# Performance work log

Measured on AMD Instinct MI355X. Metric: run time of the kernel, lower is better.

## Reference

```python
import jax, jax.numpy as jnp
import numpy as np

N_SKILL = 50000
B = 4096          # number of (job, resume) pairs; n_job == n_resume required by the concat
E = 65536         # edges per relation (avg degree 16)
D = 1536          # embedding_dim
HID = [512, 256, 64]


def setup_inputs() -> dict:
    key = jax.random.key(0)
    ks = jax.random.split(key, 16)
    nrm = lambda k, shape, s=0.02: jax.random.normal(k, shape, dtype=jnp.float32) * s
    inp = {
        "x_skill": jax.random.normal(ks[0], (N_SKILL, D), dtype=jnp.float32),
        "x_job": jax.random.normal(ks[1], (B, D), dtype=jnp.float32),
        "x_resume": jax.random.normal(ks[2], (B, D), dtype=jnp.float32),
        "src_sj": jax.random.randint(ks[3], (E,), 0, N_SKILL),
        "dst_sj": jax.random.randint(ks[4], (E,), 0, B),
        "src_sr": jax.random.randint(ks[5], (E,), 0, N_SKILL),
        "dst_sr": jax.random.randint(ks[6], (E,), 0, B),
        "W_rel_j": nrm(ks[7], (D, D)),
        "b_rel_j": jnp.zeros((D,), jnp.float32),
        "W_root_j": nrm(ks[8], (D, D)),
        "W_rel_r": nrm(ks[9], (D, D)),
        "b_rel_r": jnp.zeros((D,), jnp.float32),
        "W_root_r": nrm(ks[10], (D, D)),
        "W1": nrm(ks[11], (2 * D, HID[0])), "b1": jnp.zeros((HID[0],), jnp.float32),
        "W2": nrm(ks[12], (HID[0], HID[1])), "b2": jnp.zeros((HID[1],), jnp.float32),
        "W3": nrm(ks[13], (HID[1], HID[2])), "b3": jnp.zeros((HID[2],), jnp.float32),
        "W4": nrm(ks[14], (HID[2], 1)), "b4": jnp.zeros((1,), jnp.float32),
    }
    return inp


def _graph_conv(x_src, x_dst, src, dst, W_rel, b_rel, W_root):
    # PyG GraphConv (aggr='add', bipartite): out = lin_rel(sum_{j in N(i)} x_j) + lin_root(x_i)
    agg = jax.ops.segment_sum(x_src[src], dst, num_segments=x_dst.shape[0])  # [B, D]
    return agg @ W_rel + b_rel + x_dst @ W_root


def reference(x_skill, x_job, x_resume, src_sj, dst_sj, src_sr, dst_sr,
              W_rel_j, b_rel_j, W_root_j, W_rel_r, b_rel_r, W_root_r,
              W1, b1, W2, b2, W3, b3, W4, b4):
    # HeteroConv: each dst node type ('job', 'resume') receives exactly one relation,
    # so the cross-relation 'mean' aggregation is the identity.
    h_job = jax.nn.relu(_graph_conv(x_skill, x_job, src_sj, dst_sj, W_rel_j, b_rel_j, W_root_j))
    h_res = jax.nn.relu(_graph_conv(x_skill, x_resume, src_sr, dst_sr, W_rel_r, b_rel_r, W_root_r))
    h = jnp.concatenate([h_job, h_res], axis=1)  # [B, 2D]
    # MLP (dropout is inference-mode identity)
    h = jax.nn.relu(h @ W1 + b1)
    h = jax.nn.relu(h @ W2 + b2)
    h = jax.nn.relu(h @ W3 + b3)
    score = (h @ W4 + b4).squeeze(-1)  # [B]
    return score
```

## Files before the change

### kernel.cpp

```cpp
#include <hip/hip_runtime.h>

#define E_EDGES 65536
#define NB 4096
#define DD 1536
#define CAP 96

typedef unsigned short u16;
typedef __bf16 bf16x8 __attribute__((ext_vector_type(8)));
typedef float f32x4 __attribute__((ext_vector_type(4)));

#define AS1(p) ((const __attribute__((address_space(1))) void*)(p))
#define AS3(p) ((__attribute__((address_space(3))) void*)(p))

__device__ __forceinline__ u16 f2bf(float f) {
    unsigned u = __float_as_uint(f);
    u += 0x7fffu + ((u >> 16) & 1u);
    return (u16)(u >> 16);
}


__global__ __launch_bounds__(256) void bucket_kernel(
    const int* __restrict__ sj, const int* __restrict__ dj,
    const int* __restrict__ sr, const int* __restrict__ dr,
    int* __restrict__ cnt, int* __restrict__ bkt) {
    int e = blockIdx.x * 256 + threadIdx.x;
    int rel = blockIdx.y;
    int s = rel ? sr[e] : sj[e];
    int d = rel ? dr[e] : dj[e];
    int slot = rel * NB + d;
    int pos = atomicAdd(&cnt[slot], 1);
    if (pos < CAP) bkt[(size_t)slot * CAP + pos] = s;
}


__global__ __launch_bounds__(128) void agg_cvt_kernel(
    const float* __restrict__ xskill, const float* __restrict__ xj, const float* __restrict__ xr,
    const int* __restrict__ bkt, const int* __restrict__ cnt,
    u16* __restrict__ Aj, u16* __restrict__ Ar) {
    int rel = blockIdx.y;
    int row = blockIdx.x;
    int t = threadIdx.x;
    const float* xd = (rel ? xr : xj) + (size_t)row * DD;
    u16* A = (rel ? Ar : Aj) + (size_t)row * (2 * DD);

    float4 v[3];
#pragma unroll
    for (int c = 0; c < 3; ++c) v[c] = *(const float4*)(xd + t * 4 + c * 512);
#pragma unroll
    for (int c = 0; c < 3; ++c) {
        ushort4 o = {f2bf(v[c].x), f2bf(v[c].y), f2bf(v[c].z), f2bf(v[c].w)};
        *(ushort4*)(A + DD + t * 4 + c * 512) = o;
    }

    int count = cnt[rel * NB + row];
    if (count > CAP) count = CAP;
    __shared__ int sidx[CAP];
    if (t < count) sidx[t] = bkt[(size_t)(rel * NB + row) * CAP + t];
    __syncthreads();

    float4 acc[3] = {};
    for (int e = 0; e < count; ++e) {
        const float* xs = xskill + (size_t)sidx[e] * DD;
#pragma unroll
        for (int c = 0; c < 3; ++c) {
            float4 u = *(const float4*)(xs + t * 4 + c * 512);
            acc[c].x += u.x; acc[c].y += u.y; acc[c].z += u.z; acc[c].w += u.w;
        }
    }
#pragma unroll
    for (int c = 0; c < 3; ++c) {
        ushort4 o = {f2bf(acc[c].x), f2bf(acc[c].y), f2bf(acc[c].z), f2bf(acc[c].w)};
        *(ushort4*)(A + t * 4 + c * 512) = o;
    }
}


__global__ __launch_bounds__(256) void transpose_all(
    const float* __restrict__ w0, const float* __restrict__ w1,
    const float* __restrict__ w2, const float* __restrict__ w3,
    const float* __restrict__ w4, const float* __restrict__ w5,
    u16* __restrict__ Wjt, u16* __restrict__ Wrt,
    u16* __restrict__ W1t, u16* __restrict__ W2t) {
    int bid = blockIdx.x;
    const float* in; u16* out; int N, ldo, k0, nbx;
    if (bid < 9216) {
        int m = bid / 2304;
        bid = bid % 2304;
        in = (m == 0) ? w0 : (m == 1) ? w1 : (m == 2) ? w2 : w3;
        out = (m < 2) ? Wjt : Wrt;
        N = 1536; ldo = 3072; k0 = (m & 1) ? DD : 0; nbx = 48;
    } else if (bid < 10752) {
        bid -= 9216;
        in = w4; out = W1t; N = 512; ldo = 3072; k0 = 0; nbx = 16;
    } else {
        bid -= 10752;
        in = w5; out = W2t; N = 256; ldo = 512; k0 = 0; nbx = 8;
    }
    int bx = (bid % nbx) * 32;
    int by = (bid / nbx) * 32;
    __shared__ float tile[32][33];
    int tx = threadIdx.x & 31, ty = threadIdx.x >> 5;
#pragma unroll
    for (int i = 0; i < 4; ++i)
        tile[ty + i * 8][tx] = in[(size_t)(by + ty + i * 8) * N + bx + tx];
    __syncthreads();
#pragma unroll
    for (int i = 0; i < 4; ++i) {
        int n = bx + ty + i * 8;
        int k = by + tx;
        out[(size_t)n * ldo + k0 + k] = f2bf(tile[tx][ty + i * 8]);
    }
}


template <int BM, bool OUT_BF16, bool DUAL>
__global__ __launch_bounds__(256) void gemm_bias_relu(
    const u16* __restrict__ A0, const u16* __restrict__ Bt0, const float* __restrict__ bias0,
    const u16* __restrict__ A1, const u16* __restrict__ Bt1, const float* __restrict__ bias1,
    void* __restrict__ C, int K, int ldc) {
    constexpr int BK = 64;
    constexpr int MI = BM / 32;
    constexpr int NITER = (BM + 128) / 32;
    __shared__ u16 lA[BM * BK];
    __shared__ u16 lB[128 * BK];
    int tid = threadIdx.x;
    int lane = tid & 63;
    int w = tid >> 6;
    long bm = (long)blockIdx.x * BM;
    long bn = (long)blockIdx.y * 128;
    const u16* A = A0; const u16* Bt = Bt0; const float* bias = bias0;
    long col_ofs = 0;
    if (DUAL && blockIdx.z) { A = A1; Bt = Bt1; bias = bias1; col_ofs = DD; }
    int wm = (w >> 1) * (BM / 2), wn = (w & 1) * 64;
    f32x4 acc[MI][4] = {};
    const int lrow = lane & 15;
    const int lko = (lane >> 4) * 8;

    for (int k0 = 0; k0 < K; k0 += BK) {
#pragma unroll
        for (int i = 0; i < NITER; ++i) {
            int chunk = i * 256 + tid;
            int row = chunk >> 3, kc = chunk & 7;
            if (row < BM) {
                const u16* g = A + (bm + row) * (long)K + k0 + kc * 8;
                __builtin_amdgcn_global_load_lds(AS1(g), AS3((char*)lA + i * 4096 + w * 1024), 16, 0, 0);
            } else {
                const u16* g = Bt + (bn + row - BM) * (long)K + k0 + kc * 8;
                __builtin_amdgcn_global_load_lds(AS1(g), AS3((char*)lB + i * 4096 + w * 1024 - BM * 128), 16, 0, 0);
            }
        }
        __syncthreads();
#pragma unroll
        for (int kk = 0; kk < BK; kk += 32) {
            bf16x8 af[MI], bfr[4];
#pragma unroll
            for (int i = 0; i < MI; ++i)
                af[i] = *(const bf16x8*)(lA + (wm + i * 16 + lrow) * BK + kk + lko);
#pragma unroll
            for (int j = 0; j < 4; ++j)
                bfr[j] = *(const bf16x8*)(lB + (wn + j * 16 + lrow) * BK + kk + lko);
#pragma unroll
            for (int i = 0; i < MI; ++i)
#pragma unroll
                for (int j = 0; j < 4; ++j)
                    acc[i][j] = __builtin_amdgcn_mfma_f32_16x16x32_bf16(af[i], bfr[j], acc[i][j], 0, 0, 0);
        }
        __syncthreads();
    }

    int rb = (lane >> 4) * 4, cl = lane & 15;
#pragma unroll
    for (int i = 0; i < MI; ++i)
#pragma unroll
        for (int j = 0; j < 4; ++j) {
            long row = bm + wm + i * 16 + rb;
            long col = bn + wn + j * 16 + cl;
            float b = bias[col];
#pragma unroll
            for (int r = 0; r < 4; ++r) {
                float v = fmaxf(acc[i][j][r] + b, 0.f);
                long o = (row + r) * (long)ldc + col_ofs + col;
                if (OUT_BF16)
                    ((u16*)C)[o] = f2bf(v);
                else
                    ((float*)C)[o] = v;
            }
        }
}


__global__ __launch_bounds__(64) void l34_kernel(
    const float* __restrict__ h2, const float* __restrict__ W3, const float* __restrict__ b3,
    const float* __restrict__ W4, const float* __restrict__ b4, float* __restrict__ out) {
    int t = threadIdx.x;
    __shared__ float hrow[256];
    float w4t = W4[t];
    float b3t = b3[t];
    for (int rr = 0; rr < 4; ++rr) {
        int row = blockIdx.x * 4 + rr;
        __syncthreads();
        ((float4*)hrow)[t] = ((const float4*)(h2 + (size_t)row * 256))[t];
        __syncthreads();
        float acc = b3t;
#pragma unroll 8
        for (int k = 0; k < 256; ++k) acc = fmaf(hrow[k], W3[k * 64 + t], acc);
        acc = fmaxf(acc, 0.f);
        float s = acc * w4t;
#pragma unroll
        for (int o = 32; o > 0; o >>= 1) s += __shfl_down(s, o);
        if (t == 0) out[row] = s + b4[0];
    }
}


extern "C" void kernel_launch(void* const* d_in, const int* in_sizes, int n_in,
                              void* d_out, int out_size, void* d_ws, size_t ws_size,
                              hipStream_t stream) {
    (void)in_sizes; (void)n_in; (void)out_size; (void)ws_size;
    const float* x_skill  = (const float*)d_in[0];
    const float* x_job    = (const float*)d_in[1];
    const float* x_resume = (const float*)d_in[2];
    const int* src_sj = (const int*)d_in[3];
    const int* dst_sj = (const int*)d_in[4];
    const int* src_sr = (const int*)d_in[5];
    const int* dst_sr = (const int*)d_in[6];
    const float* W_rel_j  = (const float*)d_in[7];
    const float* b_rel_j  = (const float*)d_in[8];
    const float* W_root_j = (const float*)d_in[9];
    const float* W_rel_r  = (const float*)d_in[10];
    const float* b_rel_r  = (const float*)d_in[11];
    const float* W_root_r = (const float*)d_in[12];
    const float* W1 = (const float*)d_in[13];
    const float* b1 = (const float*)d_in[14];
    const float* W2 = (const float*)d_in[15];
    const float* b2 = (const float*)d_in[16];
    const float* W3 = (const float*)d_in[17];
    const float* b3 = (const float*)d_in[18];
    const float* W4 = (const float*)d_in[19];
    const float* b4 = (const float*)d_in[20];
    float* out = (float*)d_out;

    char* p = (char*)d_ws;
    auto alloc = [&](size_t bytes) -> char* {
        char* r = p;
        p += (bytes + 255) & ~(size_t)255;
        return r;
    };
    int* cnt = (int*)alloc(2 * NB * 4);
    int* bkt = (int*)alloc((size_t)2 * NB * CAP * 4);
    u16* Aj   = (u16*)alloc((size_t)NB * 2 * DD * 2);
    u16* Ar   = (u16*)alloc((size_t)NB * 2 * DD * 2);
    u16* Wjt  = (u16*)alloc((size_t)DD * 2 * DD * 2);
    u16* Wrt  = (u16*)alloc((size_t)DD * 2 * DD * 2);
    u16* W1t  = (u16*)alloc((size_t)512 * 3072 * 2);
    u16* W2t  = (u16*)alloc((size_t)256 * 512 * 2);
    u16* hcat = (u16*)alloc((size_t)NB * 3072 * 2);
    u16* h1   = (u16*)alloc((size_t)NB * 512 * 2);
    float* h2 = (float*)alloc((size_t)NB * 256 * 4);

    hipMemsetAsync(cnt, 0, 2 * NB * 4, stream);
    bucket_kernel<<<dim3(E_EDGES / 256, 2), 256, 0, stream>>>(src_sj, dst_sj, src_sr, dst_sr, cnt, bkt);
    transpose_all<<<10880, 256, 0, stream>>>(W_rel_j, W_root_j, W_rel_r, W_root_r, W1, W2,
                                             Wjt, Wrt, W1t, W2t);
    agg_cvt_kernel<<<dim3(NB, 2), 128, 0, stream>>>(x_skill, x_job, x_resume, bkt, cnt, Aj, Ar);

    gemm_bias_relu<128, true, true><<<dim3(NB / 128, DD / 128, 2), 256, 0, stream>>>(
        Aj, Wjt, b_rel_j, Ar, Wrt, b_rel_r, hcat, 3072, 3072);
    gemm_bias_relu<64, true, false><<<dim3(NB / 64, 512 / 128, 1), 256, 0, stream>>>(
        hcat, W1t, b1, nullptr, nullptr, nullptr, h1, 3072, 512);
    gemm_bias_relu<64, false, false><<<dim3(NB / 64, 256 / 128, 1), 256, 0, stream>>>(
        h1, W2t, b2, nullptr, nullptr, nullptr, h2, 512, 256);
    l34_kernel<<<NB / 4, 64, 0, stream>>>(h2, W3, b3, W4, b4, out);
}
```

Before: 366.2 us.

## Replace dual conv GEMM with 256x256-tile double-buffered pipelined kernel

Adds a dedicated conv GEMM kernel that uses 256x256 output tiles with 8 waves, double-buffered LDS staging, an XOR-swizzled LDS layout to avoid bank conflicts, and interleaved prefetch of the next K tile between MFMA phases using explicit vmcnt waits and barriers. It also remaps block IDs for better L2 locality. The goal is more data reuse per tile and overlap of global loads with the MFMAs in the dominant GEMM. In exchange it uses 128KB of LDS per block and many barriers, which limits occupancy and makes correctness depend on the hand-written waitcnt and barrier ordering.

```diff
diff --git a/kernel.cpp b/kernel.cpp
--- a/kernel.cpp
+++ b/kernel.cpp
@@ -11,6 +11,10 @@
 
 #define AS1(p) ((const __attribute__((address_space(1))) void*)(p))
 #define AS3(p) ((__attribute__((address_space(3))) void*)(p))
+
+#define BAR() do { __builtin_amdgcn_s_barrier(); asm volatile("" ::: "memory"); } while (0)
+#define VMCNT2() asm volatile("s_waitcnt vmcnt(2)" ::: "memory")
+#define VMCNT0() asm volatile("s_waitcnt vmcnt(0)" ::: "memory")
 
 __device__ __forceinline__ u16 f2bf(float f) {
     unsigned u = __float_as_uint(f);
@@ -113,10 +117,153 @@
 }
 
 
-template <int BM, bool OUT_BF16, bool DUAL>
+__global__ __launch_bounds__(512, 2) void conv_gemm256(
+    const u16* __restrict__ Aj, const u16* __restrict__ Wjt, const float* __restrict__ bj,
+    const u16* __restrict__ Ar, const u16* __restrict__ Wrt, const float* __restrict__ br,
+    u16* __restrict__ C) {
+    constexpr int K = 3072, NT = K / 64, LDC = 3072;
+    __shared__ u16 lds[65536];
+    int tid = threadIdx.x;
+    int lane = tid & 63;
+    int w = tid >> 6;
+
+    int bid = blockIdx.y * 16 + blockIdx.x;
+    bid = (bid & 7) * 12 + (bid >> 3);
+    long bm = (long)(bid % 16) * 256;
+    long bn = (long)(bid / 16) * 256;
+
+    const u16* A; const u16* Bt; const float* bias; long cofs;
+    if (blockIdx.z) { A = Ar; Bt = Wrt; bias = br; cofs = DD; }
+    else            { A = Aj; Bt = Wjt; bias = bj; cofs = 0;  }
+
+    int wm = (w >> 2) * 128;
+    int wn = (w & 3) * 64;
+
+    const int sr0 = (w * 2) * 8 + (lane >> 3);
+    const int sr1 = (w * 2 + 1) * 8 + (lane >> 3);
+    const int skf = ((lane & 7) * 8) ^ ((lane >> 3) << 3);
+
+    auto stageA = [&](int b, int h, long k0) {
+        const u16* g0 = A + (bm + h * 128 + sr0) * (long)K + k0 + skf;
+        const u16* g1 = A + (bm + h * 128 + sr1) * (long)K + k0 + skf;
+        __builtin_amdgcn_global_load_lds(AS1(g0), AS3(lds + b * 32768 + h * 8192 + (w * 2 + 0) * 512), 16, 0, 0);
+        __builtin_amdgcn_global_load_lds(AS1(g1), AS3(lds + b * 32768 + h * 8192 + (w * 2 + 1) * 512), 16, 0, 0);
+    };
+    auto stageB = [&](int b, int h, long k0) {
+        const u16* g0 = Bt + (bn + h * 128 + sr0) * (long)K + k0 + skf;
+        const u16* g1 = Bt + (bn + h * 128 + sr1) * (long)K + k0 + skf;
+        __builtin_amdgcn_global_load_lds(AS1(g0), AS3(lds + b * 32768 + 16384 + h * 8192 + (w * 2 + 0) * 512), 16, 0, 0);
+        __builtin_amdgcn_global_load_lds(AS1(g1), AS3(lds + b * 32768 + 16384 + h * 8192 + (w * 2 + 1) * 512), 16, 0, 0);
+    };
+
+    const int lrow = lane & 15;
+    const int lko = (lane >> 4) * 8;
+    const int rsw = (lane & 7) << 3;
+
+    auto ldA = [&](int b, int mi, int kk) -> bf16x8 {
+        return *(const bf16x8*)(lds + b * 32768 + (wm + mi * 16 + lrow) * 64 + ((kk + lko) ^ rsw));
+    };
+    auto ldB = [&](int b, int nj, int kk) -> bf16x8 {
+        return *(const bf16x8*)(lds + b * 32768 + 16384 + (wn + nj * 16 + lrow) * 64 + ((kk + lko) ^ rsw));
+    };
+
+    f32x4 acc[8][4] = {};
+    bf16x8 bfr[4];
+
+    stageA(0, 0, 0); stageA(0, 1, 0);
+    stageB(0, 0, 0); stageB(0, 1, 0);
+
+    for (int t = 0; t < NT; ++t) {
+        int b = t & 1;
+        long k1 = (long)(t + 1) * 64;
+        bool pf = (t + 1 < NT);
+
+        if (pf) { stageA(b ^ 1, 0, k1); VMCNT2(); } else { VMCNT0(); }
+        BAR();
+        {
+            bf16x8 af[4];
+#pragma unroll
+            for (int mi = 0; mi < 4; ++mi) af[mi] = ldA(b, mi, 0);
+#pragma unroll
+            for (int nj = 0; nj < 4; ++nj) bfr[nj] = ldB(b, nj, 0);
+            __builtin_amdgcn_s_setprio(1);
+#pragma unroll
+            for (int mi = 0; mi < 4; ++mi)
+#pragma unroll
+                for (int nj = 0; nj < 4; ++nj)
+                    acc[mi][nj] = __builtin_amdgcn_mfma_f32_16x16x32_bf16(af[mi], bfr[nj], acc[mi][nj], 0, 0, 0);
+            __builtin_amdgcn_s_setprio(0);
+        }
+        BAR();
+        {
+            bf16x8 af[4];
+#pragma unroll
+            for (int mi = 0; mi < 4; ++mi) af[mi] = ldA(b, 4 + mi, 0);
+            if (pf) stageA(b ^ 1, 1, k1);
+            BAR();
+            __builtin_amdgcn_s_setprio(1);
+#pragma unroll
+            for (int mi = 0; mi < 4; ++mi)
+#pragma unroll
+                for (int nj = 0; nj < 4; ++nj)
+                    acc[4 + mi][nj] = __builtin_amdgcn_mfma_f32_16x16x32_bf16(af[mi], bfr[nj], acc[4 + mi][nj], 0, 0, 0);
+            __builtin_amdgcn_s_setprio(0);
+        }
+        BAR();
+        {
+            bf16x8 af[4];
+#pragma unroll
+            for (int mi = 0; mi < 4; ++mi) af[mi] = ldA(b, mi, 32);
+#pragma unroll
+            for (int nj = 0; nj < 4; ++nj) bfr[nj] = ldB(b, nj, 32);
+            if (pf) stageB(b ^ 1, 0, k1);
+            BAR();
+            __builtin_amdgcn_s_setprio(1);
+#pragma unroll
+            for (int mi = 0; mi < 4; ++mi)
+#pragma unroll
+                for (int nj = 0; nj < 4; ++nj)
+                    acc[mi][nj] = __builtin_amdgcn_mfma_f32_16x16x32_bf16(af[mi], bfr[nj], acc[mi][nj], 0, 0, 0);
+            __builtin_amdgcn_s_setprio(0);
+        }
+        BAR();
+        {
+            bf16x8 af[4];
+#pragma unroll
+            for (int mi = 0; mi < 4; ++mi) af[mi] = ldA(b, 4 + mi, 32);
+            if (pf) stageB(b ^ 1, 1, k1);
+            BAR();
+            __builtin_amdgcn_s_setprio(1);
+#pragma unroll
+            for (int mi = 0; mi < 4; ++mi)
+#pragma unroll
+                for (int nj = 0; nj < 4; ++nj)
+                    acc[4 + mi][nj] = __builtin_amdgcn_mfma_f32_16x16x32_bf16(af[mi], bfr[nj], acc[4 + mi][nj], 0, 0, 0);
+            __builtin_amdgcn_s_setprio(0);
+        }
+        BAR();
+    }
+
+    int rb = (lane >> 4) * 4, cl = lane & 15;
+#pragma unroll
+    for (int mi = 0; mi < 8; ++mi)
+#pragma unroll
+        for (int nj = 0; nj < 4; ++nj) {
+            long row = bm + wm + mi * 16 + rb;
+            long col = bn + wn + nj * 16 + cl;
+            float bb = bias[col];
+#pragma unroll
+            for (int r = 0; r < 4; ++r) {
+                float v = fmaxf(acc[mi][nj][r] + bb, 0.f);
+                C[(row + r) * (long)LDC + cofs + col] = f2bf(v);
+            }
+        }
+}
+
+
+template <int BM, bool OUT_BF16>
 __global__ __launch_bounds__(256) void gemm_bias_relu(
-    const u16* __restrict__ A0, const u16* __restrict__ Bt0, const float* __restrict__ bias0,
-    const u16* __restrict__ A1, const u16* __restrict__ Bt1, const float* __restrict__ bias1,
+    const u16* __restrict__ A, const u16* __restrict__ Bt, const float* __restrict__ bias,
     void* __restrict__ C, int K, int ldc) {
     constexpr int BK = 64;
     constexpr int MI = BM / 32;
@@ -128,9 +275,6 @@
     int w = tid >> 6;
     long bm = (long)blockIdx.x * BM;
     long bn = (long)blockIdx.y * 128;
-    const u16* A = A0; const u16* Bt = Bt0; const float* bias = bias0;
-    long col_ofs = 0;
-    if (DUAL && blockIdx.z) { A = A1; Bt = Bt1; bias = bias1; col_ofs = DD; }
     int wm = (w >> 1) * (BM / 2), wn = (w & 1) * 64;
     f32x4 acc[MI][4] = {};
     const int lrow = lane & 15;
@@ -179,7 +323,7 @@
 #pragma unroll
             for (int r = 0; r < 4; ++r) {
                 float v = fmaxf(acc[i][j][r] + b, 0.f);
-                long o = (row + r) * (long)ldc + col_ofs + col;
+                long o = (row + r) * (long)ldc + col;
                 if (OUT_BF16)
                     ((u16*)C)[o] = f2bf(v);
                 else
@@ -264,11 +408,8 @@
                                              Wjt, Wrt, W1t, W2t);
     agg_cvt_kernel<<<dim3(NB, 2), 128, 0, stream>>>(x_skill, x_job, x_resume, bkt, cnt, Aj, Ar);
 
-    gemm_bias_relu<128, true, true><<<dim3(NB / 128, DD / 128, 2), 256, 0, stream>>>(
-        Aj, Wjt, b_rel_j, Ar, Wrt, b_rel_r, hcat, 3072, 3072);
-    gemm_bias_relu<64, true, false><<<dim3(NB / 64, 512 / 128, 1), 256, 0, stream>>>(
-        hcat, W1t, b1, nullptr, nullptr, nullptr, h1, 3072, 512);
-    gemm_bias_relu<64, false, false><<<dim3(NB / 64, 256 / 128, 1), 256, 0, stream>>>(
-        h1, W2t, b2, nullptr, nullptr, nullptr, h2, 512, 256);
+    conv_gemm256<<<dim3(16, 6, 2), 512, 0, stream>>>(Aj, Wjt, b_rel_j, Ar, Wrt, b_rel_r, hcat);
+    gemm_bias_relu<64, true><<<dim3(NB / 64, 512 / 128), 256, 0, stream>>>(hcat, W1t, b1, h1, 3072, 512);
+    gemm_bias_relu<64, false><<<dim3(NB / 64, 256 / 128), 256, 0, stream>>>(h1, W2t, b2, h2, 512, 256);
     l34_kernel<<<NB / 4, 64, 0, stream>>>(h2, W3, b3, W4, b4, out);
 }
```

New measurement: 363.7 us. Within noise of the previous version (-0.7%).
